# Optimization experiments

Hardware: AMD Instinct MI355X
Metric: run time of the kernel (lower is better)

The kernel has to match this reference:

```python
import jax, jax.numpy as jnp
import numpy as np

N = 100_000      # nodes
E = 1_600_000    # edges
NG = 512         # graphs in batch
EPS = 1e-5


def _prop(x, src, dst, n, add_self_loops):
    """GCN-normalized sparse propagation: agg_i = sum_{j->i} d_j^-1/2 d_i^-1/2 x_j."""
    ones = jnp.ones(src.shape[0], x.dtype)
    deg = jax.ops.segment_sum(ones, dst, num_segments=n)
    if add_self_loops:
        deg = deg + 1.0
    dinv = jnp.where(deg > 0, jax.lax.rsqrt(jnp.maximum(deg, 1e-12)), 0.0)
    w = dinv[src] * dinv[dst]                       # [E]
    agg = jax.ops.segment_sum(x[src] * w[:, None], dst, num_segments=n)
    if add_self_loops:
        agg = agg + x * (dinv * dinv)[:, None]
    return agg


def setup_inputs() -> dict:
    key = jax.random.key(0)
    ks = jax.random.split(key, 24)
    w = lambda k, s: jax.random.normal(k, s, jnp.float32) * 0.05
    dim = 100
    return {
        "x": jax.random.normal(ks[0], (N, 128), jnp.float32),
        "src": jax.random.randint(ks[1], (E,), 0, N),
        "dst": jax.random.randint(ks[2], (E,), 0, N),
        "batch": jnp.sort(jax.random.randint(ks[3], (N,), 0, NG)),
        # SGConv 1 & 2 (propagate then Linear)
        "W1": w(ks[4], (128, dim)), "b1": jnp.zeros((dim,), jnp.float32),
        "W2": w(ks[5], (dim, dim)), "b2": jnp.zeros((dim,), jnp.float32),
        # BatchNorm1d affine params
        "gamma": jnp.ones((dim,), jnp.float32), "beta": jnp.zeros((dim,), jnp.float32),
        # ARMAConv (num_stacks=1, num_layers=1)
        "Wa_init": w(ks[6], (dim, dim)), "Wa_root": w(ks[7], (dim, dim)),
        "ba": jnp.zeros((dim,), jnp.float32),
        # MLP head
        "Wf1": w(ks[8], (dim, 2 * dim)), "bf1": jnp.zeros((2 * dim,), jnp.float32),
        "Wf2": w(ks[9], (2 * dim, 3 * dim)), "bf2": jnp.zeros((3 * dim,), jnp.float32),
        "Wf3": w(ks[10], (3 * dim, 2 * dim)), "bf3": jnp.zeros((2 * dim,), jnp.float32),
        "Wf4": w(ks[11], (2 * dim, 1)), "bf4": jnp.zeros((1,), jnp.float32),
    }


def reference(x, src, dst, batch, W1, b1, W2, b2, gamma, beta,
              Wa_init, Wa_root, ba, Wf1, bf1, Wf2, bf2, Wf3, bf3, Wf4, bf4):
    n = x.shape[0]
    # SGConv (K=1): propagate with self-loop gcn_norm, then linear; ReLU
    h = jax.nn.relu(_prop(x, src, dst, n, True) @ W1 + b1)
    h = jax.nn.relu(_prop(h, src, dst, n, True) @ W2 + b2)
    # BatchNorm1d (training mode: batch statistics, biased var)
    mu = jnp.mean(h, axis=0)
    var = jnp.mean((h - mu) ** 2, axis=0)
    h = (h - mu) * jax.lax.rsqrt(var + EPS) * gamma + beta
    # ARMAConv (1 stack, 1 layer): ReLU(A_hat (h W_init) + h W_root + b), no self-loops
    a = jax.nn.relu(_prop(h @ Wa_init, src, dst, n, False) + h @ Wa_root + ba)
    # global_add_pool over graph ids
    g = jax.ops.segment_sum(a, batch, num_segments=NG)   # [NG, dim]
    # MLP head
    g = jax.nn.relu(g @ Wf1 + bf1)
    g = jax.nn.relu(g @ Wf2 + bf2)
    g = jax.nn.relu(g @ Wf3 + bf3)
    return g @ Wf4 + bf4
```

## Files before the change

kernel.cpp:

```cpp
#include <hip/hip_runtime.h>
#include <hip/hip_fp16.h>

#define NNODES 100000
#define NEDGES 1600000
#define NGRAPH 512
#define DIM    100
#define DP     128
#define EPSBN  1e-5f
#define NBUK   ((NNODES + 255) >> 8)
#define BINCH  8192

typedef _Float16 half8 __attribute__((ext_vector_type(8)));
typedef float floatx4 __attribute__((ext_vector_type(4)));

__global__ __launch_bounds__(256) void bin_count_kernel(const int* __restrict__ dst,
                                                        int* __restrict__ btotal, int e) {
    __shared__ int lc[NBUK];
    int tid = threadIdx.x;
    int base = blockIdx.x * BINCH;
    int m = e - base; if (m > BINCH) m = BINCH;
    for (int b = tid; b < NBUK; b += 256) lc[b] = 0;
    __syncthreads();
    for (int j = tid; j < m; j += 256)
        atomicAdd(&lc[dst[base + j] >> 8], 1);
    __syncthreads();
    for (int b = tid; b < NBUK; b += 256)
        if (lc[b]) atomicAdd(&btotal[b], lc[b]);
}

__global__ void bucket_scan_kernel(const int* __restrict__ btotal, int* __restrict__ bbase,
                                   int* __restrict__ bcursor, int e) {
    __shared__ int s[512];
    int tid = threadIdx.x;
    int v = (tid < NBUK) ? btotal[tid] : 0;
    s[tid] = v; __syncthreads();
    for (int o = 1; o < 512; o <<= 1) {
        int t = (tid >= o) ? s[tid - o] : 0;
        __syncthreads();
        s[tid] += t;
        __syncthreads();
    }
    if (tid < NBUK) {
        int base = s[tid] - v;
        bbase[tid] = base;
        bcursor[tid] = base;
    }
    if (tid == 0) bbase[NBUK] = e;
}

__global__ __launch_bounds__(256) void bin_kernel(
        const int* __restrict__ src, const int* __restrict__ dst,
        int* __restrict__ bcursor, int2* __restrict__ gpairs, int e) {
    __shared__ int2 lpairs[BINCH];
    __shared__ int lcount[NBUK], lstart[NBUK], lcur[NBUK], gbase[NBUK];
    int tid = threadIdx.x;
    int base = blockIdx.x * BINCH;
    int m = e - base; if (m > BINCH) m = BINCH;

    for (int b = tid; b < NBUK; b += 256) lcount[b] = 0;
    __syncthreads();
    for (int j = tid; j < m; j += 256)
        atomicAdd(&lcount[dst[base + j] >> 8], 1);
    __syncthreads();
    if (tid == 0) {
        int acc = 0;
        for (int b = 0; b < NBUK; b++) {
            lstart[b] = acc;
            lcur[b] = acc;
            acc += lcount[b];
        }
    }
    __syncthreads();
    for (int b = tid; b < NBUK; b += 256)
        gbase[b] = atomicAdd(&bcursor[b], lcount[b]);
    for (int j = tid; j < m; j += 256) {
        int s = src[base + j], d = dst[base + j];
        int p = atomicAdd(&lcur[d >> 8], 1);
        lpairs[p] = make_int2(s, d);
    }
    __syncthreads();
    for (int j = tid; j < m; j += 256) {
        int2 pr = lpairs[j];
        int b = pr.y >> 8;
        gpairs[gbase[b] + (j - lstart[b])] = pr;
    }
}

__global__ __launch_bounds__(256) void bucket_build_kernel(
        const int2* __restrict__ gpairs, const int* __restrict__ bbase,
        int* __restrict__ off, int* __restrict__ ssorted,
        float* __restrict__ dsl, float* __restrict__ dnsl, int n, int e) {
    __shared__ int cnt[256];
    __shared__ int sc[256];
    int b = blockIdx.x, tid = threadIdx.x;
    int node0 = b << 8;
    int e0 = bbase[b], e1 = bbase[b + 1];

    cnt[tid] = 0;
    __syncthreads();
    for (int j = e0 + tid; j < e1; j += 256)
        atomicAdd(&cnt[gpairs[j].y & 255], 1);
    __syncthreads();

    int c = cnt[tid];
    sc[tid] = c; __syncthreads();
    for (int o = 1; o < 256; o <<= 1) {
        int t = (tid >= o) ? sc[tid - o] : 0;
        __syncthreads();
        sc[tid] += t;
        __syncthreads();
    }
    int excl = sc[tid] - c;

    int node = node0 + tid;
    if (node < n) {
        off[node] = e0 + excl;
        float cf = (float)c;
        dsl[node] = rsqrtf(cf + 1.0f);
        dnsl[node] = (c > 0) ? rsqrtf(cf) : 0.0f;
    }
    if (b == NBUK - 1 && tid == 0) off[n] = e;

    __syncthreads();
    cnt[tid] = e0 + excl;
    __syncthreads();
    for (int j = e0 + tid; j < e1; j += 256) {
        int2 pr = gpairs[j];
        int p = atomicAdd(&cnt[pr.y & 255], 1);
        ssorted[p] = pr.x;
    }
}

__global__ void prescale_kernel(const float* __restrict__ x, const float* __restrict__ d,
                                __half* __restrict__ yh, int n) {
    long i = (long)blockIdx.x * blockDim.x + threadIdx.x;
    if (i >= (long)n * 32) return;
    int row = (int)(i >> 5);
    float s = d[row];
    float4 v = ((const float4*)x)[i];
    __half2 p01 = __floats2half2_rn(v.x * s, v.y * s);
    __half2 p23 = __floats2half2_rn(v.z * s, v.w * s);
    uint2 u;
    u.x = *(unsigned int*)&p01;
    u.y = *(unsigned int*)&p23;
    ((uint2*)yh)[i] = u;
}

__global__ void packW4_kernel(const float* __restrict__ W1, const float* __restrict__ W2,
                              const float* __restrict__ W3, const float* __restrict__ W4,
                              _Float16* __restrict__ Wt1, _Float16* __restrict__ Wt2,
                              _Float16* __restrict__ Wt3, _Float16* __restrict__ Wt4) {
    int which = blockIdx.x >> 6;
    int idx = (blockIdx.x & 63) * 256 + threadIdx.x;
    const float* W = (which == 0) ? W1 : (which == 1) ? W2 : (which == 2) ? W3 : W4;
    _Float16* Wt  = (which == 0) ? Wt1 : (which == 1) ? Wt2 : (which == 2) ? Wt3 : Wt4;
    int K = (which == 0) ? 128 : DIM;
    int j = idx & 7;
    int l = (idx >> 3) & 63;
    int c = idx >> 9;
    int t = c >> 2, k0 = c & 3;
    int nn = t * 16 + (l & 15);
    int k = k0 * 32 + (l >> 4) * 8 + j;
    float v = (k < K && nn < DIM) ? W[k * DIM + nn] : 0.f;
    if (which == 0) v = (k < 128 && nn < DIM) ? W[k * DIM + nn] : 0.f;
    Wt[idx] = (_Float16)v;
}

__global__ __launch_bounds__(256) void prop_kernel(
        const __half* __restrict__ pre, const int* __restrict__ ssorted,
        const int* __restrict__ off, const float* __restrict__ dinv,
        __half* __restrict__ outH, int n, int selfloop) {
    int wave = (blockIdx.x * blockDim.x + threadIdx.x) >> 6;
    int lane = threadIdx.x & 63;
    if (wave >= n) return;
    int e0 = off[wave], e1 = off[wave + 1];
    int deg = e1 - e0;
    int g = lane >> 4;
    int q = lane & 15;

    float acc[8];
#pragma unroll
    for (int i = 0; i < 8; i++) acc[i] = 0.f;

    auto addu = [&](uint4 u) {
        float2 f;
        f = __half22float2(*(__half2*)&u.x); acc[0] += f.x; acc[1] += f.y;
        f = __half22float2(*(__half2*)&u.y); acc[2] += f.x; acc[3] += f.y;
        f = __half22float2(*(__half2*)&u.z); acc[4] += f.x; acc[5] += f.y;
        f = __half22float2(*(__half2*)&u.w); acc[6] += f.x; acc[7] += f.y;
    };
    auto rowptr = [&](int s) -> const uint4* {
        return (const uint4*)&pre[(long)s * DP + q * 8];
    };

    for (int base = 0; base < deg; base += 64) {
        int m = deg - base; if (m > 64) m = 64;
        int sidx = (lane < m) ? ssorted[e0 + base + lane] : 0;
        int j = 0;
        for (; j + 16 <= m; j += 16) {
            int s0 = __shfl(sidx, j + g);
            int s1 = __shfl(sidx, j + 4 + g);
            int s2 = __shfl(sidx, j + 8 + g);
            int s3 = __shfl(sidx, j + 12 + g);
            uint4 u0 = *rowptr(s0);
            uint4 u1 = *rowptr(s1);
            uint4 u2 = *rowptr(s2);
            uint4 u3 = *rowptr(s3);
            addu(u0); addu(u1); addu(u2); addu(u3);
        }
        for (; j + 4 <= m; j += 4) {
            int s = __shfl(sidx, j + g);
            addu(*rowptr(s));
        }
        if (j < m) {
            int r = m - j;
            int s = __shfl(sidx, (g < r) ? j + g : j);
            if (g < r) addu(*rowptr(s));
        }
    }

#pragma unroll
    for (int i = 0; i < 8; i++) {
        acc[i] += __shfl_xor(acc[i], 16);
        acc[i] += __shfl_xor(acc[i], 32);
    }

    if (g == 0) {
        float dn = dinv[wave];
        if (selfloop) addu(*rowptr(wave));
        __half2 p0 = __floats2half2_rn(dn * acc[0], dn * acc[1]);
        __half2 p1 = __floats2half2_rn(dn * acc[2], dn * acc[3]);
        __half2 p2 = __floats2half2_rn(dn * acc[4], dn * acc[5]);
        __half2 p3 = __floats2half2_rn(dn * acc[6], dn * acc[7]);
        uint4 u;
        u.x = *(unsigned int*)&p0;
        u.y = *(unsigned int*)&p1;
        u.z = *(unsigned int*)&p2;
        u.w = *(unsigned int*)&p3;
        *(uint4*)&outH[(long)wave * DP + q * 8] = u;
    }
}

__global__ __launch_bounds__(256) void prop_arma_kernel(
        const __half* __restrict__ pre, const int* __restrict__ ssorted,
        const int* __restrict__ off, const float* __restrict__ dinv,
        const __half* __restrict__ R, __half* __restrict__ outH, int n) {
    int wave = (blockIdx.x * blockDim.x + threadIdx.x) >> 6;
    int lane = threadIdx.x & 63;
    if (wave >= n) return;
    int e0 = off[wave], e1 = off[wave + 1];
    int deg = e1 - e0;
    int g = lane >> 4;
    int q = lane & 15;

    float acc[8];
#pragma unroll
    for (int i = 0; i < 8; i++) acc[i] = 0.f;

    auto addu = [&](uint4 u) {
        float2 f;
        f = __half22float2(*(__half2*)&u.x); acc[0] += f.x; acc[1] += f.y;
        f = __half22float2(*(__half2*)&u.y); acc[2] += f.x; acc[3] += f.y;
        f = __half22float2(*(__half2*)&u.z); acc[4] += f.x; acc[5] += f.y;
        f = __half22float2(*(__half2*)&u.w); acc[6] += f.x; acc[7] += f.y;
    };
    auto rowptr = [&](int s) -> const uint4* {
        return (const uint4*)&pre[(long)s * DP + q * 8];
    };

    for (int base = 0; base < deg; base += 64) {
        int m = deg - base; if (m > 64) m = 64;
        int sidx = (lane < m) ? ssorted[e0 + base + lane] : 0;
        int j = 0;
        for (; j + 16 <= m; j += 16) {
            int s0 = __shfl(sidx, j + g);
            int s1 = __shfl(sidx, j + 4 + g);
            int s2 = __shfl(sidx, j + 8 + g);
            int s3 = __shfl(sidx, j + 12 + g);
            uint4 u0 = *rowptr(s0);
            uint4 u1 = *rowptr(s1);
            uint4 u2 = *rowptr(s2);
            uint4 u3 = *rowptr(s3);
            addu(u0); addu(u1); addu(u2); addu(u3);
        }
        for (; j + 4 <= m; j += 4) {
            int s = __shfl(sidx, j + g);
            addu(*rowptr(s));
        }
        if (j < m) {
            int r = m - j;
            int s = __shfl(sidx, (g < r) ? j + g : j);
            if (g < r) addu(*rowptr(s));
        }
    }

#pragma unroll
    for (int i = 0; i < 8; i++) {
        acc[i] += __shfl_xor(acc[i], 16);
        acc[i] += __shfl_xor(acc[i], 32);
    }

    if (g == 0) {
        float dn = dinv[wave];
        uint4 r4 = *(const uint4*)&R[(long)wave * DP + q * 8];
        float rr[8];
        float2 f;
        f = __half22float2(*(__half2*)&r4.x); rr[0] = f.x; rr[1] = f.y;
        f = __half22float2(*(__half2*)&r4.y); rr[2] = f.x; rr[3] = f.y;
        f = __half22float2(*(__half2*)&r4.z); rr[4] = f.x; rr[5] = f.y;
        f = __half22float2(*(__half2*)&r4.w); rr[6] = f.x; rr[7] = f.y;
        float o[8];
#pragma unroll
        for (int i = 0; i < 8; i++) o[i] = fmaxf(dn * acc[i] + rr[i], 0.f);
        __half2 p0 = __floats2half2_rn(o[0], o[1]);
        __half2 p1 = __floats2half2_rn(o[2], o[3]);
        __half2 p2 = __floats2half2_rn(o[4], o[5]);
        __half2 p3 = __floats2half2_rn(o[6], o[7]);
        uint4 u;
        u.x = *(unsigned int*)&p0;
        u.y = *(unsigned int*)&p1;
        u.z = *(unsigned int*)&p2;
        u.w = *(unsigned int*)&p3;
        *(uint4*)&outH[(long)wave * DP + q * 8] = u;
    }
}

__global__ __launch_bounds__(256) void matmul_mfma_kernel(
        const __half* __restrict__ A, const _Float16* __restrict__ WtF,
        const float* __restrict__ bias, const float* __restrict__ rowscale,
        __half* __restrict__ Ch, float* __restrict__ bnsum, float* __restrict__ bnsq,
        int M, int Kout, int relu) {
    __shared__ char smraw[64 * 132 * 4];
    _Float16* Bs = (_Float16*)smraw;
    float* Ct = (float*)smraw;
    int tid = threadIdx.x;
    int wave = tid >> 6;
    int lane = tid & 63;
    int m16 = lane & 15;
    int quad = lane >> 4;
    long row0blk = (long)blockIdx.x * 64;
    long row0 = row0blk + wave * 16;

    {
        const uint4* s = (const uint4*)WtF;
        uint4* d = (uint4*)Bs;
        for (int i = tid; i < 2048; i += 256) d[i] = s[i];
    }

    half8 af[4];
    {
        long ar = row0 + m16; if (ar >= M) ar = M - 1;
        const _Float16* Ap = (const _Float16*)&A[ar * DP + quad * 8];
#pragma unroll
        for (int k0 = 0; k0 < 4; k0++)
            af[k0] = *(const half8*)(Ap + k0 * 32);
    }
    __syncthreads();

    floatx4 acc[8];
#pragma unroll
    for (int t = 0; t < 8; t++) acc[t] = (floatx4){0.f, 0.f, 0.f, 0.f};

#pragma unroll
    for (int c = 0; c < 32; c++) {
        half8 bf = *(const half8*)&Bs[(c * 64 + lane) * 8];
        acc[c >> 2] = __builtin_amdgcn_mfma_f32_16x16x32_f16(af[c & 3], bf, acc[c >> 2], 0, 0, 0);
    }
    __syncthreads();

    int lrow0 = wave * 16 + quad * 4;
#pragma unroll
    for (int t = 0; t < 8; t++)
#pragma unroll
        for (int r = 0; r < 4; r++)
            Ct[(lrow0 + r) * 132 + t * 16 + m16] = acc[t][r];
    __syncthreads();

    float s4[4] = {0.f, 0.f, 0.f, 0.f};
    float q4[4] = {0.f, 0.f, 0.f, 0.f};
    for (int idx = tid; idx < 64 * 32; idx += 256) {
        int lr = idx >> 5, c4 = idx & 31;
        long grow = row0blk + lr;
        if (grow >= M) continue;
        int col = c4 * 4;
        float4 v = *(const float4*)&Ct[lr * 132 + col];
        if (bias && col < Kout) {
            float4 bb = *(const float4*)&bias[col];
            v.x += bb.x; v.y += bb.y; v.z += bb.z; v.w += bb.w;
        }
        if (relu) {
            v.x = fmaxf(v.x, 0.f); v.y = fmaxf(v.y, 0.f);
            v.z = fmaxf(v.z, 0.f); v.w = fmaxf(v.w, 0.f);
        }
        if (rowscale) {
            float rs = rowscale[grow];
            v.x *= rs; v.y *= rs; v.z *= rs; v.w *= rs;
        }
        if (bnsum) {
            s4[0] += v.x; s4[1] += v.y; s4[2] += v.z; s4[3] += v.w;
            q4[0] += v.x * v.x; q4[1] += v.y * v.y; q4[2] += v.z * v.z; q4[3] += v.w * v.w;
        }
        __half2 p01 = __floats2half2_rn(v.x, v.y);
        __half2 p23 = __floats2half2_rn(v.z, v.w);
        uint2 u;
        u.x = *(unsigned int*)&p01;
        u.y = *(unsigned int*)&p23;
        *(uint2*)&Ch[grow * DP + col] = u;
    }

    if (bnsum) {
        __syncthreads();
        float* scr = Ct;
        int g = tid >> 5, c4 = tid & 31;
#pragma unroll
        for (int i = 0; i < 4; i++) {
            scr[g * 128 + c4 * 4 + i] = s4[i];
            scr[1024 + g * 128 + c4 * 4 + i] = q4[i];
        }
        __syncthreads();
        if (tid < 128) {
            float ss = 0.f, qq = 0.f;
#pragma unroll
            for (int gg = 0; gg < 8; gg++) {
                ss += scr[gg * 128 + tid];
                qq += scr[1024 + gg * 128 + tid];
            }
            atomicAdd(&bnsum[tid], ss);
            atomicAdd(&bnsq[tid], qq);
        }
    }
}

__global__ __launch_bounds__(256) void matmul_dual_kernel(
        const __half* __restrict__ A, const _Float16* __restrict__ WtF3,
        const _Float16* __restrict__ WtF4, const float* __restrict__ ba,
        const float* __restrict__ rowscale,
        const float* __restrict__ bnscale, const float* __restrict__ bnshift,
        __half* __restrict__ Ch1, __half* __restrict__ ChR, int M, int Kout) {
    __shared__ char smraw[64 * 132 * 4];
    _Float16* Bs = (_Float16*)smraw;
    float* Ct = (float*)smraw;
    int tid = threadIdx.x;
    int wave = tid >> 6;
    int lane = tid & 63;
    int m16 = lane & 15;
    int quad = lane >> 4;
    long row0blk = (long)blockIdx.x * 64;
    long row0 = row0blk + wave * 16;

    half8 af[4];
    {
        long ar = row0 + m16; if (ar >= M) ar = M - 1;
        const _Float16* Ap = (const _Float16*)&A[ar * DP + quad * 8];
#pragma unroll
        for (int k0 = 0; k0 < 4; k0++) {
            half8 h = *(const half8*)(Ap + k0 * 32);
            int c0 = quad * 8 + k0 * 32;
            float4 sc0 = *(const float4*)&bnscale[c0];
            float4 sc1 = *(const float4*)&bnscale[c0 + 4];
            float4 sh0 = *(const float4*)&bnshift[c0];
            float4 sh1 = *(const float4*)&bnshift[c0 + 4];
            half8 o;
            o[0] = (_Float16)((float)h[0] * sc0.x + sh0.x);
            o[1] = (_Float16)((float)h[1] * sc0.y + sh0.y);
            o[2] = (_Float16)((float)h[2] * sc0.z + sh0.z);
            o[3] = (_Float16)((float)h[3] * sc0.w + sh0.w);
            o[4] = (_Float16)((float)h[4] * sc1.x + sh1.x);
            o[5] = (_Float16)((float)h[5] * sc1.y + sh1.y);
            o[6] = (_Float16)((float)h[6] * sc1.z + sh1.z);
            o[7] = (_Float16)((float)h[7] * sc1.w + sh1.w);
            af[k0] = o;
        }
    }

    floatx4 acc3[8], acc4[8];
#pragma unroll
    for (int t = 0; t < 8; t++) {
        acc3[t] = (floatx4){0.f, 0.f, 0.f, 0.f};
        acc4[t] = (floatx4){0.f, 0.f, 0.f, 0.f};
    }

    {
        const uint4* s = (const uint4*)WtF3;
        uint4* d = (uint4*)Bs;
        for (int i = tid; i < 2048; i += 256) d[i] = s[i];
    }
    __syncthreads();
#pragma unroll
    for (int c = 0; c < 32; c++) {
        half8 bf = *(const half8*)&Bs[(c * 64 + lane) * 8];
        acc3[c >> 2] = __builtin_amdgcn_mfma_f32_16x16x32_f16(af[c & 3], bf, acc3[c >> 2], 0, 0, 0);
    }
    __syncthreads();

    {
        const uint4* s = (const uint4*)WtF4;
        uint4* d = (uint4*)Bs;
        for (int i = tid; i < 2048; i += 256) d[i] = s[i];
    }
    __syncthreads();
#pragma unroll
    for (int c = 0; c < 32; c++) {
        half8 bf = *(const half8*)&Bs[(c * 64 + lane) * 8];
        acc4[c >> 2] = __builtin_amdgcn_mfma_f32_16x16x32_f16(af[c & 3], bf, acc4[c >> 2], 0, 0, 0);
    }
    __syncthreads();

    int lrow0 = wave * 16 + quad * 4;

#pragma unroll
    for (int t = 0; t < 8; t++)
#pragma unroll
        for (int r = 0; r < 4; r++)
            Ct[(lrow0 + r) * 132 + t * 16 + m16] = acc3[t][r];
    __syncthreads();
    for (int idx = tid; idx < 64 * 32; idx += 256) {
        int lr = idx >> 5, c4 = idx & 31;
        long grow = row0blk + lr;
        if (grow >= M) continue;
        int col = c4 * 4;
        float4 v = *(const float4*)&Ct[lr * 132 + col];
        float rs = rowscale[grow];
        v.x *= rs; v.y *= rs; v.z *= rs; v.w *= rs;
        __half2 p01 = __floats2half2_rn(v.x, v.y);
        __half2 p23 = __floats2half2_rn(v.z, v.w);
        uint2 u;
        u.x = *(unsigned int*)&p01;
        u.y = *(unsigned int*)&p23;
        *(uint2*)&Ch1[grow * DP + col] = u;
    }
    __syncthreads();

#pragma unroll
    for (int t = 0; t < 8; t++)
#pragma unroll
        for (int r = 0; r < 4; r++)
            Ct[(lrow0 + r) * 132 + t * 16 + m16] = acc4[t][r];
    __syncthreads();
    for (int idx = tid; idx < 64 * 32; idx += 256) {
        int lr = idx >> 5, c4 = idx & 31;
        long grow = row0blk + lr;
        if (grow >= M) continue;
        int col = c4 * 4;
        float4 v = *(const float4*)&Ct[lr * 132 + col];
        if (col < Kout) {
            float4 bb = *(const float4*)&ba[col];
            v.x += bb.x; v.y += bb.y; v.z += bb.z; v.w += bb.w;
        }
        __half2 p01 = __floats2half2_rn(v.x, v.y);
        __half2 p23 = __floats2half2_rn(v.z, v.w);
        uint2 u;
        u.x = *(unsigned int*)&p01;
        u.y = *(unsigned int*)&p23;
        *(uint2*)&ChR[grow * DP + col] = u;
    }
}

__global__ void bn_prep_kernel(const float* __restrict__ sum, const float* __restrict__ sq,
                               const float* __restrict__ gamma, const float* __restrict__ beta,
                               float* __restrict__ scale, float* __restrict__ shift, int n) {
    int c = threadIdx.x;
    float sc = 0.f, sh = 0.f;
    if (c < DIM) {
        float inv_n = 1.0f / (float)n;
        float mu = sum[c] * inv_n;
        float var = sq[c] * inv_n - mu * mu;
        float rs = rsqrtf(var + EPSBN);
        sc = rs * gamma[c];
        sh = beta[c] - mu * sc;
    }
    scale[c] = sc;
    shift[c] = sh;
}

__global__ void gbounds_kernel(const int* __restrict__ batch, int* __restrict__ gstart, int n) {
    int g = threadIdx.x;
    int lo = 0, hi = n;
    while (lo < hi) {
        int mid = (lo + hi) >> 1;
        if (batch[mid] < g) lo = mid + 1; else hi = mid;
    }
    gstart[g] = lo;
    if (g == 0) gstart[NGRAPH] = n;
}

__global__ __launch_bounds__(512) void pool_kernel(const __half* __restrict__ a,
                                                   const int* __restrict__ gstart,
                                                   float* __restrict__ g) {
    __shared__ float2 red[512];
    int b = blockIdx.x, tid = threadIdx.x;
    int col2 = tid & 63;
    int rgrp = tid >> 6;
    int lo = gstart[b], hi = gstart[b + 1];
    float2 s = make_float2(0.f, 0.f);
    for (int r = lo + rgrp; r < hi; r += 8) {
        __half2 h = *(const __half2*)&a[(long)r * DP + col2 * 2];
        float2 f = __half22float2(h);
        s.x += f.x; s.y += f.y;
    }
    red[tid] = s;
    __syncthreads();
    if (tid < 64) {
        float2 t = make_float2(0.f, 0.f);
#pragma unroll
        for (int gg = 0; gg < 8; gg++) {
            float2 v = red[gg * 64 + tid];
            t.x += v.x; t.y += v.y;
        }
        *(float2*)&g[b * DP + tid * 2] = t;
    }
}

__global__ __launch_bounds__(256) void mlp_kernel(
        const float* __restrict__ g,
        const float* __restrict__ Wf1, const float* __restrict__ bf1,
        const float* __restrict__ Wf2, const float* __restrict__ bf2,
        const float* __restrict__ Wf3, const float* __restrict__ bf3,
        const float* __restrict__ Wf4, const float* __restrict__ bf4,
        float* __restrict__ out) {
    __shared__ float a0[100], a1[200], a2[300], a3[200], red[256];
    int b = blockIdx.x, tid = threadIdx.x;
    if (tid < 100) a0[tid] = g[b * DP + tid];
    __syncthreads();
    for (int c = tid; c < 200; c += 256) {
        float s = bf1[c];
        for (int k = 0; k < 100; k++) s += a0[k] * Wf1[k * 200 + c];
        a1[c] = fmaxf(s, 0.f);
    }
    __syncthreads();
    for (int c = tid; c < 300; c += 256) {
        float s = bf2[c];
        for (int k = 0; k < 200; k++) s += a1[k] * Wf2[k * 300 + c];
        a2[c] = fmaxf(s, 0.f);
    }
    __syncthreads();
    for (int c = tid; c < 200; c += 256) {
        float s = bf3[c];
        for (int k = 0; k < 300; k++) s += a2[k] * Wf3[k * 200 + c];
        a3[c] = fmaxf(s, 0.f);
    }
    __syncthreads();
    red[tid] = (tid < 200) ? a3[tid] * Wf4[tid] : 0.f;
    __syncthreads();
    for (int o = 128; o > 0; o >>= 1) {
        if (tid < o) red[tid] += red[tid + o];
        __syncthreads();
    }
    if (tid == 0) out[b] = red[0] + bf4[0];
}

extern "C" void kernel_launch(void* const* d_in, const int* in_sizes, int n_in,
                              void* d_out, int out_size, void* d_ws, size_t ws_size,
                              hipStream_t stream) {
    const float* x      = (const float*)d_in[0];
    const int*   src    = (const int*)d_in[1];
    const int*   dst    = (const int*)d_in[2];
    const int*   batch  = (const int*)d_in[3];
    const float* W1     = (const float*)d_in[4];
    const float* b1     = (const float*)d_in[5];
    const float* W2     = (const float*)d_in[6];
    const float* b2     = (const float*)d_in[7];
    const float* gamma  = (const float*)d_in[8];
    const float* beta   = (const float*)d_in[9];
    const float* Wa_init= (const float*)d_in[10];
    const float* Wa_root= (const float*)d_in[11];
    const float* ba     = (const float*)d_in[12];
    const float* Wf1    = (const float*)d_in[13];
    const float* bf1    = (const float*)d_in[14];
    const float* Wf2    = (const float*)d_in[15];
    const float* bf2    = (const float*)d_in[16];
    const float* Wf3    = (const float*)d_in[17];
    const float* bf3    = (const float*)d_in[18];
    const float* Wf4    = (const float*)d_in[19];
    const float* bf4    = (const float*)d_in[20];
    float* out = (float*)d_out;

    const int n = NNODES;
    const int e = NEDGES;

    char* ws = (char*)d_ws;
    auto carve = [&](size_t bytes) -> void* {
        void* p = (void*)ws;
        ws += (bytes + 255) & ~(size_t)255;
        return p;
    };
    __half* bufH    = (__half*)carve((size_t)n * DP * 2);
    __half* bufHA   = (__half*)carve((size_t)n * DP * 2);
    __half* bufHB   = (__half*)carve((size_t)n * DP * 2);
    __half* bufR    = (__half*)carve((size_t)n * DP * 2);
    __half* bufHC   = (__half*)carve((size_t)n * DP * 2);
    _Float16* Wt1   = (_Float16*)carve((size_t)DP * DP * 2);
    _Float16* Wt2   = (_Float16*)carve((size_t)DP * DP * 2);
    _Float16* Wt3   = (_Float16*)carve((size_t)DP * DP * 2);
    _Float16* Wt4   = (_Float16*)carve((size_t)DP * DP * 2);
    int*    off     = (int*)carve((size_t)(n + 1) * 4);
    int*    btotal  = (int*)carve((size_t)NBUK * 4);
    int*    bbase   = (int*)carve((size_t)(NBUK + 1) * 4);
    int*    bcursor = (int*)carve((size_t)NBUK * 4);
    int*    ssorted = (int*)carve((size_t)e * 4);
    int2*   gpairs  = (int2*)carve((size_t)e * 8);
    float*  dinv_sl = (float*)carve((size_t)n * 4);
    float*  dinv_nsl= (float*)carve((size_t)n * 4);
    float*  bnsum   = (float*)carve(DP * 4);
    float*  bnsq    = (float*)carve(DP * 4);
    float*  bnscale = (float*)carve(DP * 4);
    float*  bnshift = (float*)carve(DP * 4);
    int*    gstart  = (int*)carve((size_t)(NGRAPH + 1) * 4);
    float*  gpool   = (float*)carve((size_t)NGRAPH * DP * 4);

    const int nchunk = (e + BINCH - 1) / BINCH;

    packW4_kernel<<<256, 256, 0, stream>>>(W1, W2, Wa_init, Wa_root, Wt1, Wt2, Wt3, Wt4);

    hipMemsetAsync(btotal, 0, (size_t)NBUK * 4, stream);
    hipMemsetAsync(bnsum, 0, DP * 4, stream);
    hipMemsetAsync(bnsq, 0, DP * 4, stream);
    bin_count_kernel<<<nchunk, 256, 0, stream>>>(dst, btotal, e);
    bucket_scan_kernel<<<1, 512, 0, stream>>>(btotal, bbase, bcursor, e);
    bin_kernel<<<nchunk, 256, 0, stream>>>(src, dst, bcursor, gpairs, e);
    bucket_build_kernel<<<NBUK, 256, 0, stream>>>(gpairs, bbase, off, ssorted, dinv_sl, dinv_nsl, n, e);
    gbounds_kernel<<<1, 512, 0, stream>>>(batch, gstart, n);

    const int prop_blocks = (n + 3) / 4;
    const int mm_blocks = (n + 63) / 64;

    prescale_kernel<<<(int)(((long)n * 32 + 255) / 256), 256, 0, stream>>>(x, dinv_sl, bufH, n);
    prop_kernel<<<prop_blocks, 256, 0, stream>>>(bufH, ssorted, off, dinv_sl, bufHA, n, 1);
    matmul_mfma_kernel<<<mm_blocks, 256, 0, stream>>>(bufHA, Wt1, b1, dinv_sl, bufH, nullptr, nullptr, n, DIM, 1);

    prop_kernel<<<prop_blocks, 256, 0, stream>>>(bufH, ssorted, off, dinv_sl, bufHA, n, 1);
    matmul_mfma_kernel<<<mm_blocks, 256, 0, stream>>>(bufHA, Wt2, b2, nullptr, bufHB, bnsum, bnsq, n, DIM, 1);

    bn_prep_kernel<<<1, 128, 0, stream>>>(bnsum, bnsq, gamma, beta, bnscale, bnshift, n);

    matmul_dual_kernel<<<mm_blocks, 256, 0, stream>>>(bufHB, Wt3, Wt4, ba, dinv_nsl, bnscale, bnshift, bufH, bufR, n, DIM);
    prop_arma_kernel<<<prop_blocks, 256, 0, stream>>>(bufH, ssorted, off, dinv_nsl, bufR, bufHC, n);

    pool_kernel<<<NGRAPH, 512, 0, stream>>>(bufHC, gstart, gpool);

    mlp_kernel<<<NGRAPH, 256, 0, stream>>>(gpool, Wf1, bf1, Wf2, bf2, Wf3, bf3, Wf4, bf4, out);
}
```

Baseline: 554.0 us.

## Reorder linear before propagation and shrink feature row stride to 104

Uses linearity to apply W1 and W2 before sparse propagation, so the gather runs on 100-wide outputs instead of 128-wide inputs. Bias and ReLU move into the propagation epilogue, and a separate BN-statistics pass replaces the fused reduction. Row stride drops from 128 to 104 halves, which cuts gather and stream bytes by about 19%, and the prescale kernel is removed by having the first matmul read fp32 x directly. The cost is an extra BN-stats read pass, plus idle lanes in the gather waves.

```diff
diff --git a/kernel.cpp b/kernel.cpp
--- a/kernel.cpp
+++ b/kernel.cpp
@@ -6,6 +6,8 @@
 #define NGRAPH 512
 #define DIM    100
 #define DP     128
+#define SP     104
+#define NU4    13
 #define EPSBN  1e-5f
 #define NBUK   ((NNODES + 255) >> 8)
 #define BINCH  8192
@@ -129,21 +131,6 @@
         int p = atomicAdd(&cnt[pr.y & 255], 1);
         ssorted[p] = pr.x;
     }
-}
-
-__global__ void prescale_kernel(const float* __restrict__ x, const float* __restrict__ d,
-                                __half* __restrict__ yh, int n) {
-    long i = (long)blockIdx.x * blockDim.x + threadIdx.x;
-    if (i >= (long)n * 32) return;
-    int row = (int)(i >> 5);
-    float s = d[row];
-    float4 v = ((const float4*)x)[i];
-    __half2 p01 = __floats2half2_rn(v.x * s, v.y * s);
-    __half2 p23 = __floats2half2_rn(v.z * s, v.w * s);
-    uint2 u;
-    u.x = *(unsigned int*)&p01;
-    u.y = *(unsigned int*)&p23;
-    ((uint2*)yh)[i] = u;
 }
 
 __global__ void packW4_kernel(const float* __restrict__ W1, const float* __restrict__ W2,
@@ -162,14 +149,20 @@
     int nn = t * 16 + (l & 15);
     int k = k0 * 32 + (l >> 4) * 8 + j;
     float v = (k < K && nn < DIM) ? W[k * DIM + nn] : 0.f;
-    if (which == 0) v = (k < 128 && nn < DIM) ? W[k * DIM + nn] : 0.f;
     Wt[idx] = (_Float16)v;
+}
+
+__global__ void padb_kernel(const float* __restrict__ b1, const float* __restrict__ b2,
+                            float* __restrict__ b1p, float* __restrict__ b2p) {
+    int c = threadIdx.x;
+    b1p[c] = (c < DIM) ? b1[c] : 0.f;
+    b2p[c] = (c < DIM) ? b2[c] : 0.f;
 }
 
 __global__ __launch_bounds__(256) void prop_kernel(
         const __half* __restrict__ pre, const int* __restrict__ ssorted,
         const int* __restrict__ off, const float* __restrict__ dinv,
-        __half* __restrict__ outH, int n, int selfloop) {
+        const float* __restrict__ bias, __half* __restrict__ outH, int n) {
     int wave = (blockIdx.x * blockDim.x + threadIdx.x) >> 6;
     int lane = threadIdx.x & 63;
     if (wave >= n) return;
@@ -177,6 +170,7 @@
     int deg = e1 - e0;
     int g = lane >> 4;
     int q = lane & 15;
+    bool act = q < NU4;
 
     float acc[8];
 #pragma unroll
@@ -190,7 +184,7 @@
         f = __half22float2(*(__half2*)&u.w); acc[6] += f.x; acc[7] += f.y;
     };
     auto rowptr = [&](int s) -> const uint4* {
-        return (const uint4*)&pre[(long)s * DP + q * 8];
+        return (const uint4*)&pre[(long)s * SP + q * 8];
     };
 
     for (int base = 0; base < deg; base += 64) {
@@ -202,20 +196,22 @@
             int s1 = __shfl(sidx, j + 4 + g);
             int s2 = __shfl(sidx, j + 8 + g);
             int s3 = __shfl(sidx, j + 12 + g);
-            uint4 u0 = *rowptr(s0);
-            uint4 u1 = *rowptr(s1);
-            uint4 u2 = *rowptr(s2);
-            uint4 u3 = *rowptr(s3);
-            addu(u0); addu(u1); addu(u2); addu(u3);
+            if (act) {
+                uint4 u0 = *rowptr(s0);
+                uint4 u1 = *rowptr(s1);
+                uint4 u2 = *rowptr(s2);
+                uint4 u3 = *rowptr(s3);
+                addu(u0); addu(u1); addu(u2); addu(u3);
+            }
         }
         for (; j + 4 <= m; j += 4) {
             int s = __shfl(sidx, j + g);
-            addu(*rowptr(s));
+            if (act) addu(*rowptr(s));
         }
         if (j < m) {
             int r = m - j;
             int s = __shfl(sidx, (g < r) ? j + g : j);
-            if (g < r) addu(*rowptr(s));
+            if (g < r && act) addu(*rowptr(s));
         }
     }
 
@@ -225,19 +221,30 @@
         acc[i] += __shfl_xor(acc[i], 32);
     }
 
-    if (g == 0) {
+    if (g == 0 && act) {
         float dn = dinv[wave];
-        if (selfloop) addu(*rowptr(wave));
-        __half2 p0 = __floats2half2_rn(dn * acc[0], dn * acc[1]);
-        __half2 p1 = __floats2half2_rn(dn * acc[2], dn * acc[3]);
-        __half2 p2 = __floats2half2_rn(dn * acc[4], dn * acc[5]);
-        __half2 p3 = __floats2half2_rn(dn * acc[6], dn * acc[7]);
+        addu(*rowptr(wave));
+        float4 b0 = *(const float4*)&bias[q * 8];
+        float4 b1v = *(const float4*)&bias[q * 8 + 4];
+        float o[8];
+        o[0] = fmaxf(dn * acc[0] + b0.x, 0.f);
+        o[1] = fmaxf(dn * acc[1] + b0.y, 0.f);
+        o[2] = fmaxf(dn * acc[2] + b0.z, 0.f);
+        o[3] = fmaxf(dn * acc[3] + b0.w, 0.f);
+        o[4] = fmaxf(dn * acc[4] + b1v.x, 0.f);
+        o[5] = fmaxf(dn * acc[5] + b1v.y, 0.f);
+        o[6] = fmaxf(dn * acc[6] + b1v.z, 0.f);
+        o[7] = fmaxf(dn * acc[7] + b1v.w, 0.f);
+        __half2 p0 = __floats2half2_rn(o[0], o[1]);
+        __half2 p1 = __floats2half2_rn(o[2], o[3]);
+        __half2 p2 = __floats2half2_rn(o[4], o[5]);
+        __half2 p3 = __floats2half2_rn(o[6], o[7]);
         uint4 u;
         u.x = *(unsigned int*)&p0;
         u.y = *(unsigned int*)&p1;
         u.z = *(unsigned int*)&p2;
         u.w = *(unsigned int*)&p3;
-        *(uint4*)&outH[(long)wave * DP + q * 8] = u;
+        *(uint4*)&outH[(long)wave * SP + q * 8] = u;
     }
 }
 
@@ -252,6 +259,7 @@
     int deg = e1 - e0;
     int g = lane >> 4;
     int q = lane & 15;
+    bool act = q < NU4;
 
     float acc[8];
 #pragma unroll
@@ -265,7 +273,7 @@
         f = __half22float2(*(__half2*)&u.w); acc[6] += f.x; acc[7] += f.y;
     };
     auto rowptr = [&](int s) -> const uint4* {
-        return (const uint4*)&pre[(long)s * DP + q * 8];
+        return (const uint4*)&pre[(long)s * SP + q * 8];
     };
 
     for (int base = 0; base < deg; base += 64) {
@@ -277,20 +285,22 @@
             int s1 = __shfl(sidx, j + 4 + g);
             int s2 = __shfl(sidx, j + 8 + g);
             int s3 = __shfl(sidx, j + 12 + g);
-            uint4 u0 = *rowptr(s0);
-            uint4 u1 = *rowptr(s1);
-            uint4 u2 = *rowptr(s2);
-            uint4 u3 = *rowptr(s3);
-            addu(u0); addu(u1); addu(u2); addu(u3);
+            if (act) {
+                uint4 u0 = *rowptr(s0);
+                uint4 u1 = *rowptr(s1);
+                uint4 u2 = *rowptr(s2);
+                uint4 u3 = *rowptr(s3);
+                addu(u0); addu(u1); addu(u2); addu(u3);
+            }
         }
         for (; j + 4 <= m; j += 4) {
             int s = __shfl(sidx, j + g);
-            addu(*rowptr(s));
+            if (act) addu(*rowptr(s));
         }
         if (j < m) {
             int r = m - j;
             int s = __shfl(sidx, (g < r) ? j + g : j);
-            if (g < r) addu(*rowptr(s));
+            if (g < r && act) addu(*rowptr(s));
         }
     }
 
@@ -300,9 +310,9 @@
         acc[i] += __shfl_xor(acc[i], 32);
     }
 
-    if (g == 0) {
+    if (g == 0 && act) {
         float dn = dinv[wave];
-        uint4 r4 = *(const uint4*)&R[(long)wave * DP + q * 8];
+        uint4 r4 = *(const uint4*)&R[(long)wave * SP + q * 8];
         float rr[8];
         float2 f;
         f = __half22float2(*(__half2*)&r4.x); rr[0] = f.x; rr[1] = f.y;
@@ -321,15 +331,13 @@
         u.y = *(unsigned int*)&p1;
         u.z = *(unsigned int*)&p2;
         u.w = *(unsigned int*)&p3;
-        *(uint4*)&outH[(long)wave * DP + q * 8] = u;
-    }
-}
-
-__global__ __launch_bounds__(256) void matmul_mfma_kernel(
-        const __half* __restrict__ A, const _Float16* __restrict__ WtF,
-        const float* __restrict__ bias, const float* __restrict__ rowscale,
-        __half* __restrict__ Ch, float* __restrict__ bnsum, float* __restrict__ bnsq,
-        int M, int Kout, int relu) {
+        *(uint4*)&outH[(long)wave * SP + q * 8] = u;
+    }
+}
+
+__global__ __launch_bounds__(256) void matmul_a32_kernel(
+        const float* __restrict__ A, const _Float16* __restrict__ WtF,
+        const float* __restrict__ rowscale, __half* __restrict__ Ch, int M) {
     __shared__ char smraw[64 * 132 * 4];
     _Float16* Bs = (_Float16*)smraw;
     float* Ct = (float*)smraw;
@@ -350,10 +358,18 @@
     half8 af[4];
     {
         long ar = row0 + m16; if (ar >= M) ar = M - 1;
-        const _Float16* Ap = (const _Float16*)&A[ar * DP + quad * 8];
-#pragma unroll
-        for (int k0 = 0; k0 < 4; k0++)
-            af[k0] = *(const half8*)(Ap + k0 * 32);
+        const float* Ap = &A[ar * DP + quad * 8];
+#pragma unroll
+        for (int k0 = 0; k0 < 4; k0++) {
+            float4 v0 = *(const float4*)(Ap + k0 * 32);
+            float4 v1 = *(const float4*)(Ap + k0 * 32 + 4);
+            half8 o;
+            o[0] = (_Float16)v0.x; o[1] = (_Float16)v0.y;
+            o[2] = (_Float16)v0.z; o[3] = (_Float16)v0.w;
+            o[4] = (_Float16)v1.x; o[5] = (_Float16)v1.y;
+            o[6] = (_Float16)v1.z; o[7] = (_Float16)v1.w;
+            af[k0] = o;
+        }
     }
     __syncthreads();
 
@@ -376,58 +392,95 @@
             Ct[(lrow0 + r) * 132 + t * 16 + m16] = acc[t][r];
     __syncthreads();
 
-    float s4[4] = {0.f, 0.f, 0.f, 0.f};
-    float q4[4] = {0.f, 0.f, 0.f, 0.f};
     for (int idx = tid; idx < 64 * 32; idx += 256) {
         int lr = idx >> 5, c4 = idx & 31;
         long grow = row0blk + lr;
-        if (grow >= M) continue;
         int col = c4 * 4;
+        if (grow >= M || col >= SP) continue;
         float4 v = *(const float4*)&Ct[lr * 132 + col];
-        if (bias && col < Kout) {
-            float4 bb = *(const float4*)&bias[col];
-            v.x += bb.x; v.y += bb.y; v.z += bb.z; v.w += bb.w;
-        }
-        if (relu) {
-            v.x = fmaxf(v.x, 0.f); v.y = fmaxf(v.y, 0.f);
-            v.z = fmaxf(v.z, 0.f); v.w = fmaxf(v.w, 0.f);
-        }
-        if (rowscale) {
-            float rs = rowscale[grow];
-            v.x *= rs; v.y *= rs; v.z *= rs; v.w *= rs;
-        }
-        if (bnsum) {
-            s4[0] += v.x; s4[1] += v.y; s4[2] += v.z; s4[3] += v.w;
-            q4[0] += v.x * v.x; q4[1] += v.y * v.y; q4[2] += v.z * v.z; q4[3] += v.w * v.w;
-        }
+        float rs = rowscale[grow];
+        v.x *= rs; v.y *= rs; v.z *= rs; v.w *= rs;
         __half2 p01 = __floats2half2_rn(v.x, v.y);
         __half2 p23 = __floats2half2_rn(v.z, v.w);
         uint2 u;
         u.x = *(unsigned int*)&p01;
         u.y = *(unsigned int*)&p23;
-        *(uint2*)&Ch[grow * DP + col] = u;
-    }
-
-    if (bnsum) {
-        __syncthreads();
-        float* scr = Ct;
-        int g = tid >> 5, c4 = tid & 31;
-#pragma unroll
-        for (int i = 0; i < 4; i++) {
-            scr[g * 128 + c4 * 4 + i] = s4[i];
-            scr[1024 + g * 128 + c4 * 4 + i] = q4[i];
-        }
-        __syncthreads();
-        if (tid < 128) {
-            float ss = 0.f, qq = 0.f;
-#pragma unroll
-            for (int gg = 0; gg < 8; gg++) {
-                ss += scr[gg * 128 + tid];
-                qq += scr[1024 + gg * 128 + tid];
+        *(uint2*)&Ch[grow * SP + col] = u;
+    }
+}
+
+__global__ __launch_bounds__(256) void matmul_a16_kernel(
+        const __half* __restrict__ A, const _Float16* __restrict__ WtF,
+        const float* __restrict__ rowscale, __half* __restrict__ Ch, int M) {
+    __shared__ char smraw[64 * 132 * 4];
+    _Float16* Bs = (_Float16*)smraw;
+    float* Ct = (float*)smraw;
+    int tid = threadIdx.x;
+    int wave = tid >> 6;
+    int lane = tid & 63;
+    int m16 = lane & 15;
+    int quad = lane >> 4;
+    long row0blk = (long)blockIdx.x * 64;
+    long row0 = row0blk + wave * 16;
+
+    {
+        const uint4* s = (const uint4*)WtF;
+        uint4* d = (uint4*)Bs;
+        for (int i = tid; i < 2048; i += 256) d[i] = s[i];
+    }
+
+    half8 af[4];
+    {
+        long ar = row0 + m16; if (ar >= M) ar = M - 1;
+        const _Float16* Ap = (const _Float16*)&A[ar * SP];
+#pragma unroll
+        for (int k0 = 0; k0 < 4; k0++) {
+            int c0 = quad * 8 + k0 * 32;
+            if (c0 < SP) {
+                af[k0] = *(const half8*)(Ap + c0);
+            } else {
+                half8 z;
+#pragma unroll
+                for (int jj = 0; jj < 8; jj++) z[jj] = (_Float16)0.f;
+                af[k0] = z;
             }
-            atomicAdd(&bnsum[tid], ss);
-            atomicAdd(&bnsq[tid], qq);
-        }
+        }
+    }
+    __syncthreads();
+
+    floatx4 acc[8];
+#pragma unroll
+    for (int t = 0; t < 8; t++) acc[t] = (floatx4){0.f, 0.f, 0.f, 0.f};
+
+#pragma unroll
+    for (int c = 0; c < 32; c++) {
+        half8 bf = *(const half8*)&Bs[(c * 64 + lane) * 8];
+        acc[c >> 2] = __builtin_amdgcn_mfma_f32_16x16x32_f16(af[c & 3], bf, acc[c >> 2], 0, 0, 0);
+    }
+    __syncthreads();
+
+    int lrow0 = wave * 16 + quad * 4;
+#pragma unroll
+    for (int t = 0; t < 8; t++)
+#pragma unroll
+        for (int r = 0; r < 4; r++)
+            Ct[(lrow0 + r) * 132 + t * 16 + m16] = acc[t][r];
+    __syncthreads();
+
+    for (int idx = tid; idx < 64 * 32; idx += 256) {
+        int lr = idx >> 5, c4 = idx & 31;
+        long grow = row0blk + lr;
+        int col = c4 * 4;
+        if (grow >= M || col >= SP) continue;
+        float4 v = *(const float4*)&Ct[lr * 132 + col];
+        float rs = rowscale[grow];
+        v.x *= rs; v.y *= rs; v.z *= rs; v.w *= rs;
+        __half2 p01 = __floats2half2_rn(v.x, v.y);
+        __half2 p23 = __floats2half2_rn(v.z, v.w);
+        uint2 u;
+        u.x = *(unsigned int*)&p01;
+        u.y = *(unsigned int*)&p23;
+        *(uint2*)&Ch[grow * SP + col] = u;
     }
 }
 
@@ -451,24 +504,29 @@
     half8 af[4];
     {
         long ar = row0 + m16; if (ar >= M) ar = M - 1;
-        const _Float16* Ap = (const _Float16*)&A[ar * DP + quad * 8];
+        const _Float16* Ap = (const _Float16*)&A[ar * SP];
 #pragma unroll
         for (int k0 = 0; k0 < 4; k0++) {
-            half8 h = *(const half8*)(Ap + k0 * 32);
             int c0 = quad * 8 + k0 * 32;
-            float4 sc0 = *(const float4*)&bnscale[c0];
-            float4 sc1 = *(const float4*)&bnscale[c0 + 4];
-            float4 sh0 = *(const float4*)&bnshift[c0];
-            float4 sh1 = *(const float4*)&bnshift[c0 + 4];
             half8 o;
-            o[0] = (_Float16)((float)h[0] * sc0.x + sh0.x);
-            o[1] = (_Float16)((float)h[1] * sc0.y + sh0.y);
-            o[2] = (_Float16)((float)h[2] * sc0.z + sh0.z);
-            o[3] = (_Float16)((float)h[3] * sc0.w + sh0.w);
-            o[4] = (_Float16)((float)h[4] * sc1.x + sh1.x);
-            o[5] = (_Float16)((float)h[5] * sc1.y + sh1.y);
-            o[6] = (_Float16)((float)h[6] * sc1.z + sh1.z);
-            o[7] = (_Float16)((float)h[7] * sc1.w + sh1.w);
+            if (c0 < SP) {
+                half8 h = *(const half8*)(Ap + c0);
+                float4 sc0 = *(const float4*)&bnscale[c0];
+                float4 sc1 = *(const float4*)&bnscale[c0 + 4];
+                float4 sh0 = *(const float4*)&bnshift[c0];
+                float4 sh1 = *(const float4*)&bnshift[c0 + 4];
+                o[0] = (_Float16)((float)h[0] * sc0.x + sh0.x);
+                o[1] = (_Float16)((float)h[1] * sc0.y + sh0.y);
+                o[2] = (_Float16)((float)h[2] * sc0.z + sh0.z);
+                o[3] = (_Float16)((float)h[3] * sc0.w + sh0.w);
+                o[4] = (_Float16)((float)h[4] * sc1.x + sh1.x);
+                o[5] = (_Float16)((float)h[5] * sc1.y + sh1.y);
+                o[6] = (_Float16)((float)h[6] * sc1.z + sh1.z);
+                o[7] = (_Float16)((float)h[7] * sc1.w + sh1.w);
+            } else {
+#pragma unroll
+                for (int jj = 0; jj < 8; jj++) o[jj] = (_Float16)0.f;
+            }
             af[k0] = o;
         }
     }
@@ -517,8 +575,8 @@
     for (int idx = tid; idx < 64 * 32; idx += 256) {
         int lr = idx >> 5, c4 = idx & 31;
         long grow = row0blk + lr;
-        if (grow >= M) continue;
         int col = c4 * 4;
+        if (grow >= M || col >= SP) continue;
         float4 v = *(const float4*)&Ct[lr * 132 + col];
         float rs = rowscale[grow];
         v.x *= rs; v.y *= rs; v.z *= rs; v.w *= rs;
@@ -527,7 +585,7 @@
         uint2 u;
         u.x = *(unsigned int*)&p01;
         u.y = *(unsigned int*)&p23;
-        *(uint2*)&Ch1[grow * DP + col] = u;
+        *(uint2*)&Ch1[grow * SP + col] = u;
     }
     __syncthreads();
 
@@ -540,8 +598,8 @@
     for (int idx = tid; idx < 64 * 32; idx += 256) {
         int lr = idx >> 5, c4 = idx & 31;
         long grow = row0blk + lr;
-        if (grow >= M) continue;
         int col = c4 * 4;
+        if (grow >= M || col >= SP) continue;
         float4 v = *(const float4*)&Ct[lr * 132 + col];
         if (col < Kout) {
             float4 bb = *(const float4*)&ba[col];
@@ -552,7 +610,39 @@
         uint2 u;
         u.x = *(unsigned int*)&p01;
         u.y = *(unsigned int*)&p23;
-        *(uint2*)&ChR[grow * DP + col] = u;
+        *(uint2*)&ChR[grow * SP + col] = u;
+    }
+}
+
+__global__ __launch_bounds__(512) void bnstats_kernel(const __half* __restrict__ h,
+                                                      float* __restrict__ bnsum,
+                                                      float* __restrict__ bnsq, int n) {
+    __shared__ float2 sred[512], qred[512];
+    int tid = threadIdx.x;
+    int col2 = tid & 63;
+    int rgrp = tid >> 6;
+    float2 s = make_float2(0.f, 0.f), qv = make_float2(0.f, 0.f);
+    if (col2 < 52) {
+        for (int r = blockIdx.x * 8 + rgrp; r < n; r += gridDim.x * 8) {
+            __half2 hv = *(const __half2*)&h[(long)r * SP + col2 * 2];
+            float2 f = __half22float2(hv);
+            s.x += f.x; s.y += f.y;
+            qv.x += f.x * f.x; qv.y += f.y * f.y;
+        }
+    }
+    sred[tid] = s; qred[tid] = qv;
+    __syncthreads();
+    if (tid < 52) {
+        float2 ts = make_float2(0.f, 0.f), tq = make_float2(0.f, 0.f);
+#pragma unroll
+        for (int gg = 0; gg < 8; gg++) {
+            float2 v = sred[gg * 64 + tid]; ts.x += v.x; ts.y += v.y;
+            v = qred[gg * 64 + tid]; tq.x += v.x; tq.y += v.y;
+        }
+        atomicAdd(&bnsum[tid * 2], ts.x);
+        atomicAdd(&bnsum[tid * 2 + 1], ts.y);
+        atomicAdd(&bnsq[tid * 2], tq.x);
+        atomicAdd(&bnsq[tid * 2 + 1], tq.y);
     }
 }
 
@@ -593,14 +683,16 @@
     int rgrp = tid >> 6;
     int lo = gstart[b], hi = gstart[b + 1];
     float2 s = make_float2(0.f, 0.f);
-    for (int r = lo + rgrp; r < hi; r += 8) {
-        __half2 h = *(const __half2*)&a[(long)r * DP + col2 * 2];
-        float2 f = __half22float2(h);
-        s.x += f.x; s.y += f.y;
+    if (col2 < 52) {
+        for (int r = lo + rgrp; r < hi; r += 8) {
+            __half2 h = *(const __half2*)&a[(long)r * SP + col2 * 2];
+            float2 f = __half22float2(h);
+            s.x += f.x; s.y += f.y;
+        }
     }
     red[tid] = s;
     __syncthreads();
-    if (tid < 64) {
+    if (tid < 52) {
         float2 t = make_float2(0.f, 0.f);
 #pragma unroll
         for (int gg = 0; gg < 8; gg++) {
@@ -684,11 +776,10 @@
         ws += (bytes + 255) & ~(size_t)255;
         return p;
     };
-    __half* bufH    = (__half*)carve((size_t)n * DP * 2);
-    __half* bufHA   = (__half*)carve((size_t)n * DP * 2);
-    __half* bufHB   = (__half*)carve((size_t)n * DP * 2);
-    __half* bufR    = (__half*)carve((size_t)n * DP * 2);
-    __half* bufHC   = (__half*)carve((size_t)n * DP * 2);
+    __half* buf0    = (__half*)carve((size_t)n * SP * 2);
+    __half* buf1    = (__half*)carve((size_t)n * SP * 2);
+    __half* bufR    = (__half*)carve((size_t)n * SP * 2);
+    __half* bufC    = (__half*)carve((size_t)n * SP * 2);
     _Float16* Wt1   = (_Float16*)carve((size_t)DP * DP * 2);
     _Float16* Wt2   = (_Float16*)carve((size_t)DP * DP * 2);
     _Float16* Wt3   = (_Float16*)carve((size_t)DP * DP * 2);
@@ -705,12 +796,15 @@
     float*  bnsq    = (float*)carve(DP * 4);
     float*  bnscale = (float*)carve(DP * 4);
     float*  bnshift = (float*)carve(DP * 4);
+    float*  b1p     = (float*)carve(DP * 4);
+    float*  b2p     = (float*)carve(DP * 4);
     int*    gstart  = (int*)carve((size_t)(NGRAPH + 1) * 4);
     float*  gpool   = (float*)carve((size_t)NGRAPH * DP * 4);
 
     const int nchunk = (e + BINCH - 1) / BINCH;
 
     packW4_kernel<<<256, 256, 0, stream>>>(W1, W2, Wa_init, Wa_root, Wt1, Wt2, Wt3, Wt4);
+    padb_kernel<<<1, 128, 0, stream>>>(b1, b2, b1p, b2p);
 
     hipMemsetAsync(btotal, 0, (size_t)NBUK * 4, stream);
     hipMemsetAsync(bnsum, 0, DP * 4, stream);
@@ -724,19 +818,19 @@
     const int prop_blocks = (n + 3) / 4;
     const int mm_blocks = (n + 63) / 64;
 
-    prescale_kernel<<<(int)(((long)n * 32 + 255) / 256), 256, 0, stream>>>(x, dinv_sl, bufH, n);
-    prop_kernel<<<prop_blocks, 256, 0, stream>>>(bufH, ssorted, off, dinv_sl, bufHA, n, 1);
-    matmul_mfma_kernel<<<mm_blocks, 256, 0, stream>>>(bufHA, Wt1, b1, dinv_sl, bufH, nullptr, nullptr, n, DIM, 1);
-
-    prop_kernel<<<prop_blocks, 256, 0, stream>>>(bufH, ssorted, off, dinv_sl, bufHA, n, 1);
-    matmul_mfma_kernel<<<mm_blocks, 256, 0, stream>>>(bufHA, Wt2, b2, nullptr, bufHB, bnsum, bnsq, n, DIM, 1);
-
+    matmul_a32_kernel<<<mm_blocks, 256, 0, stream>>>(x, Wt1, dinv_sl, buf0, n);
+    prop_kernel<<<prop_blocks, 256, 0, stream>>>(buf0, ssorted, off, dinv_sl, b1p, buf1, n);
+
+    matmul_a16_kernel<<<mm_blocks, 256, 0, stream>>>(buf1, Wt2, dinv_sl, buf0, n);
+    prop_kernel<<<prop_blocks, 256, 0, stream>>>(buf0, ssorted, off, dinv_sl, b2p, buf1, n);
+
+    bnstats_kernel<<<512, 512, 0, stream>>>(buf1, bnsum, bnsq, n);
     bn_prep_kernel<<<1, 128, 0, stream>>>(bnsum, bnsq, gamma, beta, bnscale, bnshift, n);
 
-    matmul_dual_kernel<<<mm_blocks, 256, 0, stream>>>(bufHB, Wt3, Wt4, ba, dinv_nsl, bnscale, bnshift, bufH, bufR, n, DIM);
-    prop_arma_kernel<<<prop_blocks, 256, 0, stream>>>(bufH, ssorted, off, dinv_nsl, bufR, bufHC, n);
-
-    pool_kernel<<<NGRAPH, 512, 0, stream>>>(bufHC, gstart, gpool);
+    matmul_dual_kernel<<<mm_blocks, 256, 0, stream>>>(buf1, Wt3, Wt4, ba, dinv_nsl, bnscale, bnshift, buf0, bufR, n, DIM);
+    prop_arma_kernel<<<prop_blocks, 256, 0, stream>>>(buf0, ssorted, off, dinv_nsl, bufR, bufC, n);
+
+    pool_kernel<<<NGRAPH, 512, 0, stream>>>(bufC, gstart, gpool);
 
     mlp_kernel<<<NGRAPH, 256, 0, stream>>>(gpool, Wf1, bf1, Wf2, bf2, Wf3, bf3, Wf4, bf4, out);
 }
```

Result: no change. 545.2 us (-1.6%).
